# Kernel tuning notes

Hardware: AMD Instinct MI355X
Metric: run time of the kernel (lower is better)

Reference implementation:

```python
import jax, jax.numpy as jnp
import numpy as np

E = 1024

def setup_inputs() -> dict:
    key = jax.random.key(0)
    ks = jax.random.split(key, 9)
    s = 1.0 / np.sqrt(E)
    return {
        "x": jax.random.normal(ks[0], (4, 2048, E), dtype=jnp.float32),
        "Wq": jax.random.uniform(ks[1], (E, E), jnp.float32, -s, s),
        "bq": jax.random.uniform(ks[2], (E,), jnp.float32, -s, s),
        "Wk": jax.random.uniform(ks[3], (E, E), jnp.float32, -s, s),
        "bk": jax.random.uniform(ks[4], (E,), jnp.float32, -s, s),
        "Wv": jax.random.uniform(ks[5], (E, E), jnp.float32, -s, s),
        "bv": jax.random.uniform(ks[6], (E,), jnp.float32, -s, s),
        "Wo": jax.random.uniform(ks[7], (E, E), jnp.float32, -s, s),
        "bo": jax.random.uniform(ks[8], (E,), jnp.float32, -s, s),
    }

def reference(x, Wq, bq, Wk, bk, Wv, bv, Wo, bo):
    # Note: the torch module never splits heads; attention is over full embed_dim.
    # nn.Linear: y = x @ W.T + b
    Q = jnp.einsum('bse,fe->bsf', x, Wq) + bq
    K = jnp.einsum('bse,fe->bsf', x, Wk) + bk
    V = jnp.einsum('bse,fe->bsf', x, Wv) + bv
    scale = 1.0 / jnp.sqrt(jnp.asarray(x.shape[-1], x.dtype))
    scores = jnp.einsum('bqe,bke->bqk', Q, K) * scale  # [B, S, S]
    weights = jax.nn.softmax(scores, axis=-1)
    out = jnp.einsum('bqk,bke->bqe', weights, V)
    # dropout is identity in eval mode
    return jnp.einsum('bse,fe->bsf', out, Wo) + bo
```

## Files before the change

kernel.cpp:

```cpp
#include <hip/hip_runtime.h>
#include <hip/hip_bf16.h>
#include <stdint.h>

typedef short bf16x8 __attribute__((ext_vector_type(8)));
typedef float f32x4 __attribute__((ext_vector_type(4)));
typedef __attribute__((address_space(3))) void lds_void_t;
typedef __attribute__((address_space(1))) void g_void_t;

static __device__ __forceinline__ unsigned short f2b(float f) {
    __hip_bfloat16 b = __float2bfloat16(f);
    return __builtin_bit_cast(unsigned short, b);
}
static __device__ __forceinline__ float b2f(unsigned int u) {
    return __builtin_bit_cast(float, u << 16);
}

__global__ __launch_bounds__(256) void prep(
    const float* __restrict__ x,
    const float* __restrict__ wq, const float* __restrict__ wk,
    const float* __restrict__ wv, const float* __restrict__ wo,
    const float* __restrict__ bq, const float* __restrict__ bk,
    const float* __restrict__ bv_, float* __restrict__ bqkv,
    ushort* __restrict__ xb, ushort* __restrict__ wqkvb)
{
    const int T = 3145728;
    int i = blockIdx.x * 256 + threadIdx.x;
    const int stride = gridDim.x * 256;
    for (; i < T; i += stride) {
        const float* src; ushort* dst; int off;
        if (i < 2097152) { src = x; dst = xb; off = i; }
        else {
            const int j = i - 2097152;
            const int w = j >> 18;
            off = j & 262143;
            src = (w == 0) ? wq : (w == 1) ? wk : (w == 2) ? wv : wo;
            dst = wqkvb + (w << 20);
        }
        float4 v = reinterpret_cast<const float4*>(src)[off];
        ushort4 o;
        o.x = f2b(v.x); o.y = f2b(v.y); o.z = f2b(v.z); o.w = f2b(v.w);
        reinterpret_cast<ushort4*>(dst)[off] = o;
    }
    const int t = blockIdx.x * 256 + threadIdx.x;
    if (t < 3072) {
        const int sec = t >> 10, of = t & 1023;
        bqkv[t] = sec == 0 ? bq[of] : (sec == 1 ? bk[of] : bv_[of]);
    }
}

template<bool HAS_BIAS>
__global__ __launch_bounds__(512, 1)
void gemm256_bt(const ushort* __restrict__ A, const ushort* __restrict__ B,
                const float* __restrict__ bias, ushort* __restrict__ C,
                ushort* __restrict__ Vt, int vtCol,
                int lda, int ldb, int ldc, int K,
                long strideA, long strideB, long strideC, float alpha)
{
    __shared__ __align__(16) ushort smem[2][2][16384];

    const int bz = blockIdx.z;
    A += (size_t)bz * strideA;
    B += (size_t)bz * strideB;
    C += (size_t)bz * strideC;

    const int gx = gridDim.x, gy = gridDim.y;
    const int nwg = gx * gy;
    int bx = blockIdx.x, by = blockIdx.y;
    if ((nwg & 7) == 0) {
        const int flat = blockIdx.x + gx * blockIdx.y;
        const int cpx = nwg >> 3;
        const int u = (flat & 7) * cpx + (flat >> 3);
        bx = u % gx;
        by = u / gx;
    }

    const int tid = threadIdx.x;
    const int w   = tid >> 6;
    const int l   = tid & 63;
    const int wr  = w >> 2;
    const int wc  = w & 3;

    const int bRow = by * 256;
    const int bCol = bx * 256;

    const int lr   = l >> 3;
    const int scol = (((l & 7) ^ lr) << 3);

    f32x4 acc[8][4];
#pragma unroll
    for (int m = 0; m < 8; ++m)
#pragma unroll
        for (int n = 0; n < 4; ++n)
            acc[m][n] = f32x4{0.f, 0.f, 0.f, 0.f};

    const int NT = K >> 6;

#pragma unroll
    for (int p = 0; p < 4; ++p) {
        const int c = w * 4 + p;
        const ushort* gA = A + (size_t)(bRow + c * 8 + lr) * lda + scol;
        const ushort* gB = B + (size_t)(bCol + c * 8 + lr) * ldb + scol;
        __builtin_amdgcn_global_load_lds((const g_void_t*)gA,
            (lds_void_t*)((char*)&smem[0][0][0] + c * 1024), 16, 0, 0);
        __builtin_amdgcn_global_load_lds((const g_void_t*)gB,
            (lds_void_t*)((char*)&smem[0][1][0] + c * 1024), 16, 0, 0);
    }

    int cur = 0;
    bf16x8 af[4][2], bfr[2][2];
    for (int t = 0; t < NT; ++t) {
        const char* sAc = (const char*)&smem[cur][0][0];
        const char* sBc = (const char*)&smem[cur][1][0];
        char* sAn = (char*)&smem[cur ^ 1][0][0];
        char* sBn = (char*)&smem[cur ^ 1][1][0];

        if (t + 1 < NT) {
            const int k1 = (t + 1) << 6;
#pragma unroll
            for (int p = 0; p < 4; ++p) {
                const int c = w * 4 + p;
                const ushort* gA = A + (size_t)(bRow + c * 8 + lr) * lda + (k1 + scol);
                const ushort* gB = B + (size_t)(bCol + c * 8 + lr) * ldb + (k1 + scol);
                __builtin_amdgcn_global_load_lds((const g_void_t*)gA,
                    (lds_void_t*)(sAn + c * 1024), 16, 0, 0);
                __builtin_amdgcn_global_load_lds((const g_void_t*)gB,
                    (lds_void_t*)(sBn + c * 1024), 16, 0, 0);
            }
            asm volatile("s_waitcnt vmcnt(8)" ::: "memory");
        } else {
            asm volatile("s_waitcnt vmcnt(0)" ::: "memory");
        }
        __builtin_amdgcn_s_barrier();
        __builtin_amdgcn_sched_barrier(0);
        asm volatile("" ::: "memory");

#pragma unroll
        for (int p = 0; p < 4; ++p) {
            const int mh = p >> 1;
            const int nh = (p == 1 || p == 2) ? 1 : 0;
            if (p == 0 || p == 2) {
#pragma unroll
                for (int i = 0; i < 4; ++i) {
                    const int ar = wr * 128 + (mh * 4 + i) * 16 + (l & 15);
#pragma unroll
                    for (int ks = 0; ks < 2; ++ks) {
                        const int slot = (ks * 4 + (l >> 4)) ^ (ar & 7);
                        af[i][ks] = *reinterpret_cast<const bf16x8*>(
                            sAc + ar * 128 + slot * 16);
                    }
                }
            }
            if (p != 2) {
#pragma unroll
                for (int j = 0; j < 2; ++j) {
                    const int br = wc * 64 + (nh * 2 + j) * 16 + (l & 15);
#pragma unroll
                    for (int ks = 0; ks < 2; ++ks) {
                        const int slot = (ks * 4 + (l >> 4)) ^ (br & 7);
                        bfr[j][ks] = *reinterpret_cast<const bf16x8*>(
                            sBc + br * 128 + slot * 16);
                    }
                }
            }
            __builtin_amdgcn_s_setprio(1);
#pragma unroll
            for (int ks = 0; ks < 2; ++ks)
#pragma unroll
                for (int i = 0; i < 4; ++i)
#pragma unroll
                    for (int j = 0; j < 2; ++j)
                        acc[mh * 4 + i][nh * 2 + j] =
                            __builtin_amdgcn_mfma_f32_16x16x32_bf16(
                                af[i][ks], bfr[j][ks],
                                acc[mh * 4 + i][nh * 2 + j], 0, 0, 0);
            __builtin_amdgcn_s_setprio(0);
        }

        asm volatile("" ::: "memory");
        __builtin_amdgcn_sched_barrier(0);
        __builtin_amdgcn_s_barrier();
        cur ^= 1;
    }

    const int cl = l & 15;
    char* stb = (char*)smem;
    if (bCol >= vtCol) {
#pragma unroll
        for (int n = 0; n < 4; ++n) {
            const int col = wc * 64 + n * 16 + cl;
            const float bv = HAS_BIAS ? bias[bCol + col] : 0.f;
#pragma unroll
            for (int m = 0; m < 8; ++m) {
                const int row0 = wr * 128 + m * 16 + (l >> 4) * 4;
#pragma unroll
                for (int r = 0; r < 4; ++r) {
                    const int row = row0 + r;
                    *(ushort*)(stb + col * 512 + ((row * 2) ^ ((col & 7) << 4))) =
                        f2b((acc[m][n][r] + bv) * alpha);
                }
            }
        }
        __syncthreads();
        const int bb    = bRow >> 11;
        const int sBase = bRow & 2047;
        const int e0    = bCol - vtCol;
        ushort* Vtb = Vt + ((size_t)bb << 21);
#pragma unroll
        for (int i = 0; i < 16; ++i) {
            const int q  = tid + (i << 9);
            const int c  = q >> 5;
            const int rq = (q & 31) << 4;
            const uint4 v = *reinterpret_cast<const uint4*>(
                stb + c * 512 + (rq ^ ((c & 7) << 4)));
            *reinterpret_cast<uint4*>(
                Vtb + (size_t)(e0 + c) * 2048 + sBase + ((q & 31) << 3)) = v;
        }
    } else {
        ushort* st = (ushort*)smem;
#pragma unroll
        for (int n = 0; n < 4; ++n) {
            const int col = wc * 64 + n * 16 + cl;
            const float bv = HAS_BIAS ? bias[bCol + col] : 0.f;
#pragma unroll
            for (int m = 0; m < 8; ++m) {
                const int row0 = wr * 128 + m * 16 + (l >> 4) * 4;
#pragma unroll
                for (int r = 0; r < 4; ++r) {
                    const int row = row0 + r;
                    const int sl  = ((col >> 3) ^ (row & 7));
                    st[row * 256 + (sl << 3) + (col & 7)] =
                        f2b((acc[m][n][r] + bv) * alpha);
                }
            }
        }
        __syncthreads();
#pragma unroll
        for (int i = 0; i < 16; ++i) {
            const int c    = tid + (i << 9);
            const int row  = c >> 5;
            const int slot = (c & 31) ^ (row & 7);
            const uint4 v = *reinterpret_cast<const uint4*>(
                (const char*)st + row * 512 + slot * 16);
            *reinterpret_cast<uint4*>(
                C + (size_t)(bRow + row) * ldc + bCol + ((c & 31) << 3)) = v;
        }
    }
}

template<typename CT, bool HAS_BIAS>
__global__ __launch_bounds__(256, 4)
void gemm_bt(const ushort* __restrict__ A, const ushort* __restrict__ B,
             const float* __restrict__ bias, CT* __restrict__ C,
             int lda, int ldb, int ldc, int K,
             long strideA, long strideB, long strideC, float alpha)
{
    __shared__ __align__(16) ushort smem[128 * 64 * 2];
    ushort* sA = smem;
    ushort* sB = smem + 128 * 64;

    const int bz = blockIdx.z;
    A += (size_t)bz * strideA;
    B += (size_t)bz * strideB;
    C += (size_t)bz * strideC;

    const int gx = gridDim.x, gy = gridDim.y;
    const int nwg = gx * gy;
    int bx = blockIdx.x, by = blockIdx.y;
    if ((nwg & 7) == 0) {
        const int flat = blockIdx.x + gx * blockIdx.y;
        const int cpx = nwg >> 3;
        const int u = (flat & 7) * cpx + (flat >> 3);
        bx = u % gx;
        by = u / gx;
    }

    const int tid = threadIdx.x;
    const int w   = tid >> 6;
    const int l   = tid & 63;
    const int wr  = w >> 1;
    const int wc  = w & 1;

    const int bRow = by * 128;
    const int bCol = bx * 128;

    const int lr   = l >> 3;
    const int scol = (((l & 7) ^ lr) << 3);

    f32x4 acc[4][4];
#pragma unroll
    for (int m = 0; m < 4; ++m)
#pragma unroll
        for (int n = 0; n < 4; ++n)
            acc[m][n] = f32x4{0.f, 0.f, 0.f, 0.f};

    for (int k0 = 0; k0 < K; k0 += 64) {
#pragma unroll
        for (int p = 0; p < 4; ++p) {
            const int c   = p * 4 + w;
            const int row = c * 8 + lr;
            const ushort* gA = A + (size_t)(bRow + row) * lda + (k0 + scol);
            const ushort* gB = B + (size_t)(bCol + row) * ldb + (k0 + scol);
            __builtin_amdgcn_global_load_lds((const g_void_t*)gA,
                (lds_void_t*)((char*)sA + c * 1024), 16, 0, 0);
            __builtin_amdgcn_global_load_lds((const g_void_t*)gB,
                (lds_void_t*)((char*)sB + c * 1024), 16, 0, 0);
        }
        __syncthreads();

        bf16x8 af[4][2], bfv[4][2];
#pragma unroll
        for (int m = 0; m < 4; ++m) {
            const int ar = wr * 64 + m * 16 + (l & 15);
#pragma unroll
            for (int ks = 0; ks < 2; ++ks) {
                const int slot = (ks * 4 + (l >> 4)) ^ (ar & 7);
                af[m][ks] = *reinterpret_cast<const bf16x8*>(
                    (const char*)sA + ar * 128 + slot * 16);
            }
        }
#pragma unroll
        for (int n = 0; n < 4; ++n) {
            const int br = wc * 64 + n * 16 + (l & 15);
#pragma unroll
            for (int ks = 0; ks < 2; ++ks) {
                const int slot = (ks * 4 + (l >> 4)) ^ (br & 7);
                bfv[n][ks] = *reinterpret_cast<const bf16x8*>(
                    (const char*)sB + br * 128 + slot * 16);
            }
        }
#pragma unroll
        for (int ks = 0; ks < 2; ++ks)
#pragma unroll
            for (int m = 0; m < 4; ++m)
#pragma unroll
                for (int n = 0; n < 4; ++n)
                    acc[m][n] = __builtin_amdgcn_mfma_f32_16x16x32_bf16(
                        af[m][ks], bfv[n][ks], acc[m][n], 0, 0, 0);
        __syncthreads();
    }

    const int cl = l & 15;
    if constexpr (sizeof(CT) == 2) {
        ushort* st = smem;
#pragma unroll
        for (int n = 0; n < 4; ++n) {
            const int col = wc * 64 + n * 16 + cl;
            const float bv = HAS_BIAS ? bias[bCol + col] : 0.f;
#pragma unroll
            for (int m = 0; m < 4; ++m) {
                const int row0 = wr * 64 + m * 16 + (l >> 4) * 4;
#pragma unroll
                for (int r = 0; r < 4; ++r)
                    st[(row0 + r) * 128 + col] = f2b((acc[m][n][r] + bv) * alpha);
            }
        }
        __syncthreads();
#pragma unroll
        for (int i = 0; i < 8; ++i) {
            const int c    = tid + i * 256;
            const int row  = c >> 4;
            const int col8 = (c & 15) * 8;
            *reinterpret_cast<uint4*>(
                (ushort*)C + (size_t)(bRow + row) * ldc + bCol + col8) =
                *reinterpret_cast<const uint4*>(st + row * 128 + col8);
        }
    } else {
#pragma unroll
        for (int n = 0; n < 4; ++n) {
            const int col = bCol + wc * 64 + n * 16 + cl;
            const float bv = HAS_BIAS ? bias[col] : 0.f;
#pragma unroll
            for (int m = 0; m < 4; ++m) {
#pragma unroll
                for (int r = 0; r < 4; ++r) {
                    const int row = bRow + wr * 64 + m * 16 + (l >> 4) * 4 + r;
                    ((float*)C)[(size_t)row * ldc + col] = (acc[m][n][r] + bv) * alpha;
                }
            }
        }
    }
}

__global__ __launch_bounds__(256) void softmax_rows(ushort* __restrict__ S)
{
    __shared__ float red[8];
    const size_t row = blockIdx.x;
    ushort* p = S + row * 2048;
    const int tid = threadIdx.x;

    uint4 v = reinterpret_cast<uint4*>(p)[tid];
    float f[8];
    const unsigned int* wv = reinterpret_cast<const unsigned int*>(&v);
#pragma unroll
    for (int j = 0; j < 4; ++j) {
        f[2 * j]     = b2f(wv[j] & 0xFFFFu);
        f[2 * j + 1] = b2f(wv[j] >> 16);
    }
    float mx = f[0];
#pragma unroll
    for (int j = 1; j < 8; ++j) mx = fmaxf(mx, f[j]);
#pragma unroll
    for (int s = 1; s < 64; s <<= 1) mx = fmaxf(mx, __shfl_xor(mx, s));
    if ((tid & 63) == 0) red[tid >> 6] = mx;
    __syncthreads();
    mx = fmaxf(fmaxf(red[0], red[1]), fmaxf(red[2], red[3]));

    float sum = 0.f;
#pragma unroll
    for (int j = 0; j < 8; ++j) { f[j] = __expf(f[j] - mx); sum += f[j]; }
#pragma unroll
    for (int s = 1; s < 64; s <<= 1) sum += __shfl_xor(sum, s);
    if ((tid & 63) == 0) red[4 + (tid >> 6)] = sum;
    __syncthreads();
    sum = (red[4] + red[5]) + (red[6] + red[7]);
    const float inv = 1.0f / sum;

    uint4 o;
    unsigned int* wo = reinterpret_cast<unsigned int*>(&o);
#pragma unroll
    for (int j = 0; j < 4; ++j) {
        const unsigned int lo = f2b(f[2 * j] * inv);
        const unsigned int hi = f2b(f[2 * j + 1] * inv);
        wo[j] = lo | (hi << 16);
    }
    reinterpret_cast<uint4*>(p)[tid] = o;
}

extern "C" void kernel_launch(void* const* d_in, const int* in_sizes, int n_in,
                              void* d_out, int out_size, void* d_ws, size_t ws_size,
                              hipStream_t stream)
{
    const float* x  = (const float*)d_in[0];
    const float* Wq = (const float*)d_in[1];
    const float* bq = (const float*)d_in[2];
    const float* Wk = (const float*)d_in[3];
    const float* bk = (const float*)d_in[4];
    const float* Wv = (const float*)d_in[5];
    const float* bv = (const float*)d_in[6];
    const float* Wo = (const float*)d_in[7];
    const float* bo = (const float*)d_in[8];

    char* ws = (char*)d_ws;
    ushort* xb    = (ushort*)(ws);
    ushort* Wqkvb = (ushort*)(ws + 16777216);
    ushort* Wob   = Wqkvb + 3 * 1048576;
    float*  bqkv  = (float*) (ws + 25165824);
    ushort* QKVb  = (ushort*)(ws + 26214400);
    ushort* Vtb   = (ushort*)(ws + 76546048);
    ushort* Sb    = (ushort*)(ws + 93323264);
    ushort* Ob    = (ushort*)(ws + 126877696);

    prep<<<2048, 256, 0, stream>>>(x, Wq, Wk, Wv, Wo, bq, bk, bv, bqkv, xb, Wqkvb);

    gemm256_bt<true><<<dim3(12, 32, 1), 512, 0, stream>>>(
        xb, Wqkvb, bqkv, QKVb, Vtb, 2048,
        1024, 1024, 3072, 1024, 0, 0, 0, 1.0f);

    gemm256_bt<false><<<dim3(8, 8, 4), 512, 0, stream>>>(
        QKVb, QKVb + 1024, nullptr, Sb, nullptr, 1 << 30,
        3072, 3072, 2048, 1024,
        2048L * 3072, 2048L * 3072, 2048L * 2048, 0.03125f);

    softmax_rows<<<8192, 256, 0, stream>>>(Sb);

    gemm_bt<ushort, false><<<dim3(8, 16, 4), 256, 0, stream>>>(
        Sb, Vtb, nullptr, Ob, 2048, 2048, 1024, 2048,
        2048L * 2048, 1024L * 2048, 2048L * 1024, 1.0f);

    gemm_bt<float, true><<<dim3(8, 64, 1), 256, 0, stream>>>(
        Ob, Wob, bo, (float*)d_out, 1024, 1024, 1024, 1024, 0, 0, 0, 1.0f);
}
```

Measured before the change: 289.2 us.

## Replace 256x256 GEMM with 256x128 triple-buffered kernel and reuse it for PV

```diff
diff --git a/kernel.cpp b/kernel.cpp
--- a/kernel.cpp
+++ b/kernel.cpp
@@ -50,13 +50,13 @@
 
 template<bool HAS_BIAS>
 __global__ __launch_bounds__(512, 1)
-void gemm256_bt(const ushort* __restrict__ A, const ushort* __restrict__ B,
-                const float* __restrict__ bias, ushort* __restrict__ C,
-                ushort* __restrict__ Vt, int vtCol,
-                int lda, int ldb, int ldc, int K,
-                long strideA, long strideB, long strideC, float alpha)
+void gemm_k3(const ushort* __restrict__ A, const ushort* __restrict__ B,
+             const float* __restrict__ bias, ushort* __restrict__ C,
+             ushort* __restrict__ Vt, int vtCol,
+             int lda, int ldb, int ldc, int K,
+             long strideA, long strideB, long strideC, float alpha)
 {
-    __shared__ __align__(16) ushort smem[2][2][16384];
+    __shared__ __align__(16) ushort smem[73728];
 
     const int bz = blockIdx.z;
     A += (size_t)bz * strideA;
@@ -77,110 +77,138 @@
     const int tid = threadIdx.x;
     const int w   = tid >> 6;
     const int l   = tid & 63;
-    const int wr  = w >> 2;
-    const int wc  = w & 3;
+    const int wr  = w >> 1;
+    const int wc  = w & 1;
 
     const int bRow = by * 256;
-    const int bCol = bx * 256;
+    const int bCol = bx * 128;
 
     const int lr   = l >> 3;
     const int scol = (((l & 7) ^ lr) << 3);
-
-    f32x4 acc[8][4];
-#pragma unroll
-    for (int m = 0; m < 8; ++m)
+    const int rowA = w * 32 + lr;
+    const int rowB = w * 16 + lr;
+
+    f32x4 acc[4][4];
+#pragma unroll
+    for (int m = 0; m < 4; ++m)
 #pragma unroll
         for (int n = 0; n < 4; ++n)
             acc[m][n] = f32x4{0.f, 0.f, 0.f, 0.f};
 
     const int NT = K >> 6;
 
-#pragma unroll
-    for (int p = 0; p < 4; ++p) {
-        const int c = w * 4 + p;
-        const ushort* gA = A + (size_t)(bRow + c * 8 + lr) * lda + scol;
-        const ushort* gB = B + (size_t)(bCol + c * 8 + lr) * ldb + scol;
-        __builtin_amdgcn_global_load_lds((const g_void_t*)gA,
-            (lds_void_t*)((char*)&smem[0][0][0] + c * 1024), 16, 0, 0);
-        __builtin_amdgcn_global_load_lds((const g_void_t*)gB,
-            (lds_void_t*)((char*)&smem[0][1][0] + c * 1024), 16, 0, 0);
-    }
-
-    int cur = 0;
-    bf16x8 af[4][2], bfr[2][2];
+#define STAGE_A(kt, rs, i)                                                      \
+    __builtin_amdgcn_global_load_lds(                                           \
+        (const g_void_t*)(A + (size_t)(bRow + rowA + (i) * 8) * lda +           \
+                          (((kt) << 6) + scol)),                                \
+        (lds_void_t*)((char*)smem + (rs) * 49152 + (w * 4 + (i)) * 1024 +       \
+                      l * 16), 16, 0, 0)
+#define STAGE_B(kt, rs, j)                                                      \
+    __builtin_amdgcn_global_load_lds(                                           \
+        (const g_void_t*)(B + (size_t)(bCol + rowB + (j) * 8) * ldb +           \
+                          (((kt) << 6) + scol)),                                \
+        (lds_void_t*)((char*)smem + (rs) * 49152 + 32768 +                      \
+                      (w * 2 + (j)) * 1024 + l * 16), 16, 0, 0)
+
+#pragma unroll
+    for (int kt = 0; kt < 2; ++kt) {
+        STAGE_A(kt, kt, 0); STAGE_A(kt, kt, 1);
+        STAGE_A(kt, kt, 2); STAGE_A(kt, kt, 3);
+        STAGE_B(kt, kt, 0); STAGE_B(kt, kt, 1);
+    }
+    asm volatile("s_waitcnt vmcnt(6)" ::: "memory");
+    __builtin_amdgcn_sched_barrier(0);
+    __builtin_amdgcn_s_barrier();
+    __builtin_amdgcn_sched_barrier(0);
+    asm volatile("" ::: "memory");
+
+    int r0 = 0;
+    bf16x8 af[2][2], bf[4][2];
     for (int t = 0; t < NT; ++t) {
-        const char* sAc = (const char*)&smem[cur][0][0];
-        const char* sBc = (const char*)&smem[cur][1][0];
-        char* sAn = (char*)&smem[cur ^ 1][0][0];
-        char* sBn = (char*)&smem[cur ^ 1][1][0];
-
-        if (t + 1 < NT) {
-            const int k1 = (t + 1) << 6;
-#pragma unroll
-            for (int p = 0; p < 4; ++p) {
-                const int c = w * 4 + p;
-                const ushort* gA = A + (size_t)(bRow + c * 8 + lr) * lda + (k1 + scol);
-                const ushort* gB = B + (size_t)(bCol + c * 8 + lr) * ldb + (k1 + scol);
-                __builtin_amdgcn_global_load_lds((const g_void_t*)gA,
-                    (lds_void_t*)(sAn + c * 1024), 16, 0, 0);
-                __builtin_amdgcn_global_load_lds((const g_void_t*)gB,
-                    (lds_void_t*)(sBn + c * 1024), 16, 0, 0);
-            }
-            asm volatile("s_waitcnt vmcnt(8)" ::: "memory");
-        } else {
-            asm volatile("s_waitcnt vmcnt(0)" ::: "memory");
-        }
+        int r2 = r0 + 2; if (r2 >= 3) r2 -= 3;
+        const char* cAb = (const char*)smem + r0 * 49152;
+        const char* cBb = cAb + 32768;
+        const bool st = (t + 2 < NT);
+        const int kt2 = t + 2;
+
+#pragma unroll
+        for (int p = 0; p < 4; ++p) {
+            const int mh = p >> 1;
+            const int nh = (p == 1 || p == 2) ? 1 : 0;
+            if (p == 0) {
+#pragma unroll
+                for (int i = 0; i < 2; ++i) {
+                    const int ar = wr * 64 + i * 16 + (l & 15);
+#pragma unroll
+                    for (int ks = 0; ks < 2; ++ks) {
+                        const int slot = (ks * 4 + (l >> 4)) ^ (ar & 7);
+                        af[i][ks] = *reinterpret_cast<const bf16x8*>(
+                            cAb + ar * 128 + slot * 16);
+                    }
+                }
+#pragma unroll
+                for (int n = 0; n < 2; ++n) {
+                    const int br = wc * 64 + n * 16 + (l & 15);
+#pragma unroll
+                    for (int ks = 0; ks < 2; ++ks) {
+                        const int slot = (ks * 4 + (l >> 4)) ^ (br & 7);
+                        bf[n][ks] = *reinterpret_cast<const bf16x8*>(
+                            cBb + br * 128 + slot * 16);
+                    }
+                }
+            } else if (p == 1) {
+#pragma unroll
+                for (int n = 2; n < 4; ++n) {
+                    const int br = wc * 64 + n * 16 + (l & 15);
+#pragma unroll
+                    for (int ks = 0; ks < 2; ++ks) {
+                        const int slot = (ks * 4 + (l >> 4)) ^ (br & 7);
+                        bf[n][ks] = *reinterpret_cast<const bf16x8*>(
+                            cBb + br * 128 + slot * 16);
+                    }
+                }
+            } else if (p == 2) {
+#pragma unroll
+                for (int i = 0; i < 2; ++i) {
+                    const int ar = wr * 64 + (2 + i) * 16 + (l & 15);
+#pragma unroll
+                    for (int ks = 0; ks < 2; ++ks) {
+                        const int slot = (ks * 4 + (l >> 4)) ^ (ar & 7);
+                        af[i][ks] = *reinterpret_cast<const bf16x8*>(
+                            cAb + ar * 128 + slot * 16);
+                    }
+                }
+            }
+            if (st) {
+                if (p == 0)      { STAGE_A(kt2, r2, 0); STAGE_B(kt2, r2, 0); }
+                else if (p == 1) { STAGE_A(kt2, r2, 1); STAGE_B(kt2, r2, 1); }
+                else if (p == 2) { STAGE_A(kt2, r2, 2); }
+                else             { STAGE_A(kt2, r2, 3); }
+            }
+            __builtin_amdgcn_s_setprio(1);
+#pragma unroll
+            for (int ks = 0; ks < 2; ++ks)
+#pragma unroll
+                for (int im = 0; im < 2; ++im)
+#pragma unroll
+                    for (int in_ = 0; in_ < 2; ++in_)
+                        acc[mh * 2 + im][nh * 2 + in_] =
+                            __builtin_amdgcn_mfma_f32_16x16x32_bf16(
+                                af[im][ks], bf[nh * 2 + in_][ks],
+                                acc[mh * 2 + im][nh * 2 + in_], 0, 0, 0);
+            __builtin_amdgcn_s_setprio(0);
+        }
+
+        if (st) asm volatile("s_waitcnt vmcnt(6)" ::: "memory");
+        else    asm volatile("s_waitcnt vmcnt(0)" ::: "memory");
+        __builtin_amdgcn_sched_barrier(0);
         __builtin_amdgcn_s_barrier();
         __builtin_amdgcn_sched_barrier(0);
         asm volatile("" ::: "memory");
-
-#pragma unroll
-        for (int p = 0; p < 4; ++p) {
-            const int mh = p >> 1;
-            const int nh = (p == 1 || p == 2) ? 1 : 0;
-            if (p == 0 || p == 2) {
-#pragma unroll
-                for (int i = 0; i < 4; ++i) {
-                    const int ar = wr * 128 + (mh * 4 + i) * 16 + (l & 15);
-#pragma unroll
-                    for (int ks = 0; ks < 2; ++ks) {
-                        const int slot = (ks * 4 + (l >> 4)) ^ (ar & 7);
-                        af[i][ks] = *reinterpret_cast<const bf16x8*>(
-                            sAc + ar * 128 + slot * 16);
-                    }
-                }
-            }
-            if (p != 2) {
-#pragma unroll
-                for (int j = 0; j < 2; ++j) {
-                    const int br = wc * 64 + (nh * 2 + j) * 16 + (l & 15);
-#pragma unroll
-                    for (int ks = 0; ks < 2; ++ks) {
-                        const int slot = (ks * 4 + (l >> 4)) ^ (br & 7);
-                        bfr[j][ks] = *reinterpret_cast<const bf16x8*>(
-                            sBc + br * 128 + slot * 16);
-                    }
-                }
-            }
-            __builtin_amdgcn_s_setprio(1);
-#pragma unroll
-            for (int ks = 0; ks < 2; ++ks)
-#pragma unroll
-                for (int i = 0; i < 4; ++i)
-#pragma unroll
-                    for (int j = 0; j < 2; ++j)
-                        acc[mh * 4 + i][nh * 2 + j] =
-                            __builtin_amdgcn_mfma_f32_16x16x32_bf16(
-                                af[i][ks], bfr[j][ks],
-                                acc[mh * 4 + i][nh * 2 + j], 0, 0, 0);
-            __builtin_amdgcn_s_setprio(0);
-        }
-
-        asm volatile("" ::: "memory");
-        __builtin_amdgcn_sched_barrier(0);
-        __builtin_amdgcn_s_barrier();
-        cur ^= 1;
-    }
+        r0 = (r0 + 1 == 3) ? 0 : r0 + 1;
+    }
+#undef STAGE_A
+#undef STAGE_B
 
     const int cl = l & 15;
     char* stb = (char*)smem;
@@ -190,8 +218,8 @@
             const int col = wc * 64 + n * 16 + cl;
             const float bv = HAS_BIAS ? bias[bCol + col] : 0.f;
 #pragma unroll
-            for (int m = 0; m < 8; ++m) {
-                const int row0 = wr * 128 + m * 16 + (l >> 4) * 4;
+            for (int m = 0; m < 4; ++m) {
+                const int row0 = wr * 64 + m * 16 + (l >> 4) * 4;
 #pragma unroll
                 for (int r = 0; r < 4; ++r) {
                     const int row = row0 + r;
@@ -206,7 +234,7 @@
         const int e0    = bCol - vtCol;
         ushort* Vtb = Vt + ((size_t)bb << 21);
 #pragma unroll
-        for (int i = 0; i < 16; ++i) {
+        for (int i = 0; i < 8; ++i) {
             const int q  = tid + (i << 9);
             const int c  = q >> 5;
             const int rq = (q & 31) << 4;
@@ -222,27 +250,27 @@
             const int col = wc * 64 + n * 16 + cl;
             const float bv = HAS_BIAS ? bias[bCol + col] : 0.f;
 #pragma unroll
-            for (int m = 0; m < 8; ++m) {
-                const int row0 = wr * 128 + m * 16 + (l >> 4) * 4;
+            for (int m = 0; m < 4; ++m) {
+                const int row0 = wr * 64 + m * 16 + (l >> 4) * 4;
 #pragma unroll
                 for (int r = 0; r < 4; ++r) {
                     const int row = row0 + r;
-                    const int sl  = ((col >> 3) ^ (row & 7));
-                    st[row * 256 + (sl << 3) + (col & 7)] =
+                    const int sl  = ((col >> 3) ^ (row & 7)) & 15;
+                    st[row * 128 + (sl << 3) + (col & 7)] =
                         f2b((acc[m][n][r] + bv) * alpha);
                 }
             }
         }
         __syncthreads();
 #pragma unroll
-        for (int i = 0; i < 16; ++i) {
+        for (int i = 0; i < 8; ++i) {
             const int c    = tid + (i << 9);
-            const int row  = c >> 5;
-            const int slot = (c & 31) ^ (row & 7);
+            const int row  = c >> 4;
+            const int slot = ((c & 15) ^ (row & 7)) & 15;
             const uint4 v = *reinterpret_cast<const uint4*>(
-                (const char*)st + row * 512 + slot * 16);
+                (const char*)st + row * 256 + slot * 16);
             *reinterpret_cast<uint4*>(
-                C + (size_t)(bRow + row) * ldc + bCol + ((c & 31) << 3)) = v;
+                C + (size_t)(bRow + row) * ldc + bCol + ((c & 15) << 3)) = v;
         }
     }
 }
@@ -452,19 +480,20 @@
 
     prep<<<2048, 256, 0, stream>>>(x, Wq, Wk, Wv, Wo, bq, bk, bv, bqkv, xb, Wqkvb);
 
-    gemm256_bt<true><<<dim3(12, 32, 1), 512, 0, stream>>>(
+    gemm_k3<true><<<dim3(24, 32, 1), 512, 0, stream>>>(
         xb, Wqkvb, bqkv, QKVb, Vtb, 2048,
         1024, 1024, 3072, 1024, 0, 0, 0, 1.0f);
 
-    gemm256_bt<false><<<dim3(8, 8, 4), 512, 0, stream>>>(
+    gemm_k3<false><<<dim3(16, 8, 4), 512, 0, stream>>>(
         QKVb, QKVb + 1024, nullptr, Sb, nullptr, 1 << 30,
         3072, 3072, 2048, 1024,
         2048L * 3072, 2048L * 3072, 2048L * 2048, 0.03125f);
 
     softmax_rows<<<8192, 256, 0, stream>>>(Sb);
 
-    gemm_bt<ushort, false><<<dim3(8, 16, 4), 256, 0, stream>>>(
-        Sb, Vtb, nullptr, Ob, 2048, 2048, 1024, 2048,
+    gemm_k3<false><<<dim3(8, 8, 4), 512, 0, stream>>>(
+        Sb, Vtb, nullptr, Ob, nullptr, 1 << 30,
+        2048, 2048, 1024, 2048,
         2048L * 2048, 1024L * 2048, 2048L * 1024, 1.0f);
 
     gemm_bt<float, true><<<dim3(8, 64, 1), 256, 0, stream>>>(
```

Result: no change. 286.2 us (-1.1%).
